# Kernel optimization log

Hardware: AMD Instinct MI355X
Metric: run time of the kernel (lower is better)

Reference implementation:

```python
import jax, jax.numpy as jnp
import numpy as np

IOU_THR = 0.5
NEG_POS = 3
CONF_W = 1.0
LOC_W = 1.0


def setup_inputs() -> dict:
    key = jax.random.key(0)
    ks = jax.random.split(key, 6)
    B, A, G = 16, 65536, 32
    ac = jax.random.uniform(ks[0], (B, A, 2))
    asz = jax.random.uniform(ks[1], (B, A, 2)) * 0.28 + 0.02
    anchors = jnp.concatenate([ac - asz / 2, ac + asz / 2], -1)
    gc = jax.random.uniform(ks[2], (B, G, 2))
    gsz = jax.random.uniform(ks[3], (B, G, 2)) * 0.28 + 0.02
    gt_boxes = jnp.concatenate([gc - gsz / 2, gc + gsz / 2], -1)
    bbox_pred = anchors + 0.05 * jax.random.normal(ks[4], (B, A, 4))
    # probabilities strictly inside (0,1) for BCE
    conf_pred = jax.random.uniform(ks[5], (B, A)) * 0.98 + 0.01
    return {"bbox_pred": bbox_pred, "conf_pred": conf_pred,
            "anchors": anchors, "gt_boxes": gt_boxes}


def _box_iou(a, g):
    # a: [A,4] xyxy, g: [G,4] xyxy -> [A,G]
    lt = jnp.maximum(a[:, None, :2], g[None, :, :2])
    rb = jnp.minimum(a[:, None, 2:], g[None, :, 2:])
    wh = jnp.clip(rb - lt, 0.0)
    inter = wh[..., 0] * wh[..., 1]
    area_a = (a[:, 2] - a[:, 0]) * (a[:, 3] - a[:, 1])
    area_g = (g[:, 2] - g[:, 0]) * (g[:, 3] - g[:, 1])
    return inter / (area_a[:, None] + area_g[None, :] - inter)


def _bce(p, t):
    return -(t * jnp.log(p) + (1.0 - t) * jnp.log1p(-p))


def _smooth_l1(x):
    ax = jnp.abs(x)
    return jnp.where(ax < 1.0, 0.5 * ax * ax, ax - 0.5)


def _per_image(bp, cp, an, gt):
    # bp: [A,4] pred boxes, cp: [A] conf, an: [A,4] anchors, gt: [G,4]
    A = cp.shape[0]
    ious = _box_iou(an, gt)                      # [A,G]
    best_gt_iou = ious.max(1)                    # [A]
    best_gt_idx = ious.argmax(1)                 # [A]
    best_anchor_idx = ious.argmax(0)             # [G] force-match each gt
    mask = (best_gt_iou > IOU_THR).at[best_anchor_idx].set(True)
    num_pos = mask.sum()

    # localization loss (center/size parameterization), summed over positives
    matched = gt[best_gt_idx]                    # [A,4]
    pc = (bp[:, :2] + bp[:, 2:]) / 2
    ps = bp[:, 2:] - bp[:, :2]
    gc = (matched[:, :2] + matched[:, 2:]) / 2
    gs = matched[:, 2:] - matched[:, :2]
    loc = _smooth_l1(jnp.concatenate([pc, ps], 1) - jnp.concatenate([gc, gs], 1)).sum(1)
    loc_loss = jnp.where(mask, loc, 0.0).sum()

    # confidence loss with hard negative mining
    t = mask.astype(cp.dtype)
    bce = _bce(cp, t)
    pos_loss = jnp.where(mask, bce, 0.0).sum()
    neg_bce = jnp.where(mask, 0.0, bce)
    num_neg = jnp.minimum(num_pos * NEG_POS, A - num_pos)
    sorted_neg = -jnp.sort(-neg_bce)             # descending
    neg_loss = jnp.where(jnp.arange(A) < num_neg, sorted_neg, 0.0).sum()
    conf_loss = pos_loss / jnp.maximum(num_pos, 1) + neg_loss / jnp.maximum(num_neg, 1)
    return loc_loss, conf_loss, num_pos


def reference(bbox_pred, conf_pred, anchors, gt_boxes):
    loc, conf, npos = jax.vmap(_per_image)(bbox_pred, conf_pred, anchors, gt_boxes)
    B = bbox_pred.shape[0]
    total_npos = jnp.maximum(npos.sum(), 1)
    total_loc = loc.sum() / total_npos * LOC_W
    total_conf = conf.sum() / B * CONF_W
    return total_loc + total_conf
```

## Files before the change

### kernel.cpp

```cpp
#include <hip/hip_runtime.h>

#define BB 16
#define AA 65536
#define GG 32
#define NB 8192
#define KOFF 59904u
#define AT 4
#define APB (256 * AT)
#define MBLK (AA / APB)
#define NSEG 16
#define SEGA (AA / NSEG)

__device__ unsigned char      g_mask[(size_t)BB * AA];
__device__ unsigned char      g_bidx[(size_t)BB * AA];
__device__ unsigned long long g_fpart[(size_t)BB * GG * MBLK];
__device__ unsigned int       g_hpart[(size_t)BB * NSEG * (NB/2)];
__device__ float g_spart[BB * NSEG * 2];
__device__ int   g_npart[BB * NSEG];
__device__ float g_loc[BB], g_pos[BB], g_neg[BB];
__device__ int   g_npos[BB], g_nneg[BB];
__device__ int   g_done;

__device__ __forceinline__ float midval(int bin) {
    return __uint_as_float((((unsigned int)bin + KOFF) << 14) | 8192u);
}

__global__ void __launch_bounds__(256, 4)
k_matchforce(const float4* __restrict__ anchors,
             const float4* __restrict__ gts) {
    __shared__ float4 sg[GG];
    __shared__ unsigned long long wkey[4][GG];
    const int b = blockIdx.y;
    const int t = threadIdx.x;
    const int wave = t >> 6, lane = t & 63;
    if (blockIdx.x == 0 && b == 0 && t == 0) g_done = 0;
    if (t < GG) sg[t] = gts[(size_t)b * GG + t];
    __syncthreads();

    const size_t abase = (size_t)b * AA + (size_t)blockIdx.x * APB;

    float ax0[AT], ay0[AT], ax1[AT], ay1[AT], aar[AT], best[AT];
    int bg[AT];
#pragma unroll
    for (int j = 0; j < AT; ++j) {
        const float4 av = anchors[abase + j * 256 + t];
        ax0[j] = av.x; ay0[j] = av.y; ax1[j] = av.z; ay1[j] = av.w;
        aar[j] = (av.z - av.x) * (av.w - av.y);
        best[j] = -1.0f; bg[j] = 0;
    }

#pragma unroll 2
    for (int g = 0; g < GG; ++g) {
        const float4 gb = sg[g];
        const float ga = (gb.z - gb.x) * (gb.w - gb.y);
        float fbest = -1.0f;
        int fo = t;
#pragma unroll
        for (int j = 0; j < AT; ++j) {
            const float lx = fmaxf(ax0[j], gb.x), ly = fmaxf(ay0[j], gb.y);
            const float rx = fminf(ax1[j], gb.z), ry = fminf(ay1[j], gb.w);
            const float w = fmaxf(rx - lx, 0.0f), h = fmaxf(ry - ly, 0.0f);
            const float inter = w * h;
            const float s = aar[j] + ga;
            const float r = inter * __builtin_amdgcn_rcpf(s);
            if (r > best[j]) { best[j] = r; bg[j] = g; }
            if (r > fbest)   { fbest = r; fo = j * 256 + t; }
        }
        unsigned long long key =
            ((unsigned long long)__float_as_uint(fbest) << 32) |
            (unsigned long long)(0xFFFFFFFFu - (unsigned int)fo);
#pragma unroll
        for (int off = 1; off < 64; off <<= 1) {
            const unsigned long long o = __shfl_xor(key, off, 64);
            if (o > key) key = o;
        }
        if (lane == 0) wkey[wave][g] = key;
    }

#pragma unroll
    for (int j = 0; j < AT; ++j) {
        g_mask[abase + j * 256 + t] = (best[j] > (1.0f / 3.0f)) ? 1 : 0;
        g_bidx[abase + j * 256 + t] = (unsigned char)bg[j];
    }
    __syncthreads();
    if (t < GG) {
        unsigned long long k = wkey[0][t];
#pragma unroll
        for (int w = 1; w < 4; ++w) {
            const unsigned long long k1 = wkey[w][t];
            if (k1 > k) k = k1;
        }
        const unsigned int off = 0xFFFFFFFFu - (unsigned int)(k & 0xFFFFFFFFull);
        const unsigned int ga = (unsigned int)(blockIdx.x * APB) + off;
        g_fpart[((size_t)b * GG + t) * MBLK + blockIdx.x] =
            (k & 0xFFFFFFFF00000000ull) |
            (unsigned long long)(0xFFFFFFFFu - ga);
    }
}

__global__ void k_stats(const float4* __restrict__ bbox,
                        const float* __restrict__ conf,
                        const float4* __restrict__ gts) {
    __shared__ float4 sg[GG];
    __shared__ unsigned int hp[NB / 2];
    __shared__ unsigned int bmap[SEGA / 32];
    __shared__ float rf[256], rf2[256];
    __shared__ unsigned int ru[256];
    const int b = blockIdx.y, seg = blockIdx.x, t = threadIdx.x;
    if (t < GG) sg[t] = gts[(size_t)b * GG + t];
    for (int j = t; j < NB / 2; j += 256) hp[j] = 0u;
    if (t < SEGA / 32) bmap[t] = 0u;
    __syncthreads();

    {
        const int gg = t >> 3, p = t & 7;
        const unsigned long long* fp =
            &g_fpart[((size_t)b * GG + gg) * MBLK + p * 8];
        unsigned long long k = 0;
#pragma unroll
        for (int m = 0; m < 8; ++m) { const unsigned long long v = fp[m]; if (v > k) k = v; }
#pragma unroll
        for (int off = 1; off < 8; off <<= 1) {
            const unsigned long long o = __shfl_xor(k, off, 64);
            if (o > k) k = o;
        }
        if (p == 0) {
            const unsigned int a = 0xFFFFFFFFu - (unsigned int)(k & 0xFFFFFFFFull);
            const int la = (int)a - seg * SEGA;
            if (la >= 0 && la < SEGA) atomicOr(&bmap[la >> 5], 1u << (la & 31));
        }
    }
    __syncthreads();

    const size_t base = (size_t)b * AA + (size_t)seg * SEGA;
    const float4* c4 = (const float4*)(conf + base);
    const uchar4* m4 = (const uchar4*)(g_mask + base);
    const uchar4* x4 = (const uchar4*)(g_bidx + base);
    const float4* bb4 = bbox + base;

    float pos = 0.0f, loc = 0.0f;
    int np = 0;
#pragma unroll
    for (int j = 0; j < SEGA / 1024; ++j) {
        const int idx = j * 256 + t;
        const float4 p4 = c4[idx];
        const uchar4 mm = m4[idx];
        const uchar4 xx = x4[idx];
        const unsigned int bw = (bmap[idx >> 3] >> ((idx & 7) * 4)) & 0xFu;
        const float pv[4] = {p4.x, p4.y, p4.z, p4.w};
        const unsigned char mv[4] = {mm.x, mm.y, mm.z, mm.w};
        const unsigned char xv[4] = {xx.x, xx.y, xx.z, xx.w};
#pragma unroll
        for (int c = 0; c < 4; ++c) {
            const float p = pv[c];
            if (mv[c] | ((bw >> c) & 1u)) {
                np += 1;
                pos += -logf(p);
                const float4 bv = bb4[4 * idx + c];
                const float4 gb = sg[xv[c]];
                const float d0 = (bv.x + bv.z) * 0.5f - (gb.x + gb.z) * 0.5f;
                const float d1 = (bv.y + bv.w) * 0.5f - (gb.y + gb.w) * 0.5f;
                const float d2 = (bv.z - bv.x) - (gb.z - gb.x);
                const float d3 = (bv.w - bv.y) - (gb.w - gb.y);
                float ds[4] = {d0, d1, d2, d3};
#pragma unroll
                for (int q = 0; q < 4; ++q) {
                    float ax = fabsf(ds[q]);
                    loc += (ax < 1.0f) ? 0.5f * ax * ax : ax - 0.5f;
                }
            } else {
                const float nb = -log1pf(-p);
                int key = (int)(__float_as_uint(nb) >> 14) - (int)KOFF;
                key = key < 0 ? 0 : (key > NB - 1 ? NB - 1 : key);
                atomicAdd(&hp[key >> 1], 1u << ((key & 1) << 4));
            }
        }
    }
    ru[t] = (unsigned int)np; rf[t] = pos; rf2[t] = loc;
    __syncthreads();
    for (int w = 128; w > 0; w >>= 1) {
        if (t < w) { ru[t] += ru[t + w]; rf[t] += rf[t + w]; rf2[t] += rf2[t + w]; }
        __syncthreads();
    }
    if (t == 0) {
        g_npart[b * NSEG + seg] = (int)ru[0];
        g_spart[(b * NSEG + seg) * 2 + 0] = rf[0];
        g_spart[(b * NSEG + seg) * 2 + 1] = rf2[0];
    }
    unsigned int* outp = g_hpart + ((size_t)b * NSEG + seg) * (NB / 2);
    for (int j = t; j < NB / 2; j += 256) outp[j] = hp[j];
}

__global__ void __launch_bounds__(1024) k_select(unsigned int* __restrict__ out) {
    __shared__ unsigned int hist[NB];
    __shared__ unsigned int ru[1024];
    __shared__ unsigned int s2[32];
    __shared__ float sh_pos, sh_loc;
    __shared__ int sh_np, sh_k, sh_bsel;
    __shared__ unsigned int sh_take;
    __shared__ float rf[1024];

    const int b = blockIdx.x, t = threadIdx.x;
    for (int w = t; w < NB / 2; w += 1024) {
        unsigned int lo = 0, hi = 0;
#pragma unroll
        for (int s = 0; s < NSEG; ++s) {
            const unsigned int v = g_hpart[((size_t)b * NSEG + s) * (NB / 2) + w];
            lo += v & 0xFFFFu; hi += v >> 16;
        }
        hist[2 * w] = lo; hist[2 * w + 1] = hi;
    }
    if (t == 0) {
        int np = 0; float pos = 0.0f, loc = 0.0f;
        for (int s = 0; s < NSEG; ++s) {
            np += g_npart[b * NSEG + s];
            pos += g_spart[(b * NSEG + s) * 2 + 0];
            loc += g_spart[(b * NSEG + s) * 2 + 1];
        }
        sh_np = np; sh_pos = pos; sh_loc = loc;
    }
    __syncthreads();
    const int np_tot = sh_np;

    unsigned int c = 0;
    const int hi = NB - 1 - t * 8;
#pragma unroll
    for (int j = 0; j < 8; ++j) c += hist[hi - j];
    ru[t] = c;
    __syncthreads();
    if (t < 32) {
        unsigned int x = 0;
#pragma unroll
        for (int j = 0; j < 32; ++j) x += ru[t * 32 + j];
        s2[t] = x;
    }
    __syncthreads();
    if (t == 0) {
        int k = 3 * np_tot;
        const int maxneg = AA - np_tot;
        if (k > maxneg) k = maxneg;
        sh_k = k;
        int bsel = NB;
        unsigned int take = 0;
        if (k > 0) {
            unsigned int cum = 0;
            int u = 0;
            while (u < 31 && cum + s2[u] < (unsigned int)k) { cum += s2[u]; ++u; }
            int cc = u * 32;
            while (cc < 1023 && cum + ru[cc] < (unsigned int)k) { cum += ru[cc]; ++cc; }
            const int h2 = NB - 1 - cc * 8;
            int j = 0;
            while (j < 7 && cum + hist[h2 - j] < (unsigned int)k) { cum += hist[h2 - j]; ++j; }
            bsel = h2 - j;
            take = (unsigned int)k - cum;
        }
        sh_bsel = bsel; sh_take = take;
    }
    __syncthreads();
    const int bsel = sh_bsel;
    float negp = 0.0f;
    for (int j = t; j < NB; j += 1024)
        if (j > bsel) { unsigned int cnt = hist[j]; if (cnt) negp += (float)cnt * midval(j); }
    rf[t] = negp;
    __syncthreads();
    for (int w = 512; w > 0; w >>= 1) {
        if (t < w) rf[t] += rf[t + w];
        __syncthreads();
    }
    if (t == 0) {
        float neg = 0.0f;
        if (sh_k > 0) neg = rf[0] + (float)sh_take * midval(bsel < NB ? bsel : 0);
        g_loc[b] = sh_loc; g_pos[b] = sh_pos; g_neg[b] = neg;
        g_npos[b] = np_tot; g_nneg[b] = sh_k;

        __threadfence();
        const int old = atomicAdd(&g_done, 1);
        if (old == BB - 1) {
            __threadfence();
            float loc = 0.0f, conf = 0.0f;
            int tot = 0;
            for (int bb = 0; bb < BB; ++bb) {
                const float lv = __hip_atomic_load(&g_loc[bb],  __ATOMIC_RELAXED, __HIP_MEMORY_SCOPE_AGENT);
                const float pv = __hip_atomic_load(&g_pos[bb],  __ATOMIC_RELAXED, __HIP_MEMORY_SCOPE_AGENT);
                const float nv = __hip_atomic_load(&g_neg[bb],  __ATOMIC_RELAXED, __HIP_MEMORY_SCOPE_AGENT);
                const int   np = __hip_atomic_load(&g_npos[bb], __ATOMIC_RELAXED, __HIP_MEMORY_SCOPE_AGENT);
                const int   nn = __hip_atomic_load(&g_nneg[bb], __ATOMIC_RELAXED, __HIP_MEMORY_SCOPE_AGENT);
                loc += lv;
                conf += pv / (float)(np > 1 ? np : 1) +
                        nv / (float)(nn > 1 ? nn : 1);
                tot += np;
            }
            const float total = loc / (float)(tot > 1 ? tot : 1) + conf / (float)BB;
            const unsigned int u = __float_as_uint(total);
            const unsigned int r = 0x7FFFu + ((u >> 16) & 1u);
            const unsigned int bf = (u + r) >> 16;
            out[0] = (bf << 16) | bf;
        }
    }
}

extern "C" void kernel_launch(void* const* d_in, const int* in_sizes, int n_in,
                              void* d_out, int out_size, void* d_ws, size_t ws_size,
                              hipStream_t stream) {
    const float4* bbox    = (const float4*)d_in[0];
    const float*  conf    = (const float*)d_in[1];
    const float4* anchors = (const float4*)d_in[2];
    const float4* gts     = (const float4*)d_in[3];

    k_matchforce<<<dim3(MBLK, BB), 256, 0, stream>>>(anchors, gts);
    k_stats<<<dim3(NSEG, BB), 256, 0, stream>>>(bbox, conf, gts);
    k_select<<<BB, 1024, 0, stream>>>((unsigned int*)d_out);
}
```

Measured before the change: 132.1 us.

## Accumulate histograms and force-match keys with global atomics, widen stats grid

Replaces the per-segment partial histograms and the per-block force-match key partials with per-image global buffers that are updated by atomicAdd and atomicMax. The buffers are zeroed by a memset issued before the kernels. k_stats now uses 64 segments, one element group per thread, instead of 16 segments with a loop, which gives more parallelism. k_select reads one finished histogram per image instead of reducing 16 partials. The aim is to remove the large partial-histogram writes and reads, at the cost of contended global atomics and an extra memset launch.

```diff
diff --git a/kernel.cpp b/kernel.cpp
--- a/kernel.cpp
+++ b/kernel.cpp
@@ -8,18 +8,27 @@
 #define AT 4
 #define APB (256 * AT)
 #define MBLK (AA / APB)
-#define NSEG 16
+#define NSEG 64
 #define SEGA (AA / NSEG)
 
-__device__ unsigned char      g_mask[(size_t)BB * AA];
-__device__ unsigned char      g_bidx[(size_t)BB * AA];
-__device__ unsigned long long g_fpart[(size_t)BB * GG * MBLK];
-__device__ unsigned int       g_hpart[(size_t)BB * NSEG * (NB/2)];
+__device__ unsigned char g_mask[(size_t)BB * AA];
+__device__ unsigned char g_bidx[(size_t)BB * AA];
 __device__ float g_spart[BB * NSEG * 2];
 __device__ int   g_npart[BB * NSEG];
 __device__ float g_loc[BB], g_pos[BB], g_neg[BB];
 __device__ int   g_npos[BB], g_nneg[BB];
-__device__ int   g_done;
+
+#define DYN_U32 (BB * NB + BB * GG * 2 + 2)
+__device__ unsigned int g_dyn[DYN_U32];
+__device__ __forceinline__ unsigned int* histp(int b) {
+    return g_dyn + (size_t)b * NB;
+}
+__device__ __forceinline__ unsigned long long* fkeyp() {
+    return (unsigned long long*)(g_dyn + BB * NB);
+}
+__device__ __forceinline__ int* donep() {
+    return (int*)(g_dyn + BB * NB + BB * GG * 2);
+}
 
 __device__ __forceinline__ float midval(int bin) {
     return __uint_as_float((((unsigned int)bin + KOFF) << 14) | 8192u);
@@ -33,7 +42,6 @@
     const int b = blockIdx.y;
     const int t = threadIdx.x;
     const int wave = t >> 6, lane = t & 63;
-    if (blockIdx.x == 0 && b == 0 && t == 0) g_done = 0;
     if (t < GG) sg[t] = gts[(size_t)b * GG + t];
     __syncthreads();
 
@@ -92,9 +100,9 @@
         }
         const unsigned int off = 0xFFFFFFFFu - (unsigned int)(k & 0xFFFFFFFFull);
         const unsigned int ga = (unsigned int)(blockIdx.x * APB) + off;
-        g_fpart[((size_t)b * GG + t) * MBLK + blockIdx.x] =
-            (k & 0xFFFFFFFF00000000ull) |
-            (unsigned long long)(0xFFFFFFFFu - ga);
+        atomicMax(&fkeyp()[b * GG + t],
+                  (k & 0xFFFFFFFF00000000ull) |
+                  (unsigned long long)(0xFFFFFFFFu - ga));
     }
 }
 
@@ -102,33 +110,18 @@
                         const float* __restrict__ conf,
                         const float4* __restrict__ gts) {
     __shared__ float4 sg[GG];
-    __shared__ unsigned int hp[NB / 2];
     __shared__ unsigned int bmap[SEGA / 32];
     __shared__ float rf[256], rf2[256];
     __shared__ unsigned int ru[256];
     const int b = blockIdx.y, seg = blockIdx.x, t = threadIdx.x;
     if (t < GG) sg[t] = gts[(size_t)b * GG + t];
-    for (int j = t; j < NB / 2; j += 256) hp[j] = 0u;
     if (t < SEGA / 32) bmap[t] = 0u;
     __syncthreads();
-
-    {
-        const int gg = t >> 3, p = t & 7;
-        const unsigned long long* fp =
-            &g_fpart[((size_t)b * GG + gg) * MBLK + p * 8];
-        unsigned long long k = 0;
-#pragma unroll
-        for (int m = 0; m < 8; ++m) { const unsigned long long v = fp[m]; if (v > k) k = v; }
-#pragma unroll
-        for (int off = 1; off < 8; off <<= 1) {
-            const unsigned long long o = __shfl_xor(k, off, 64);
-            if (o > k) k = o;
-        }
-        if (p == 0) {
-            const unsigned int a = 0xFFFFFFFFu - (unsigned int)(k & 0xFFFFFFFFull);
-            const int la = (int)a - seg * SEGA;
-            if (la >= 0 && la < SEGA) atomicOr(&bmap[la >> 5], 1u << (la & 31));
-        }
+    if (t < GG) {
+        const unsigned long long k = fkeyp()[b * GG + t];
+        const unsigned int a = 0xFFFFFFFFu - (unsigned int)(k & 0xFFFFFFFFull);
+        const int la = (int)a - seg * SEGA;
+        if (la >= 0 && la < SEGA) atomicOr(&bmap[la >> 5], 1u << (la & 31));
     }
     __syncthreads();
 
@@ -137,12 +130,12 @@
     const uchar4* m4 = (const uchar4*)(g_mask + base);
     const uchar4* x4 = (const uchar4*)(g_bidx + base);
     const float4* bb4 = bbox + base;
+    unsigned int* hb = histp(b);
 
     float pos = 0.0f, loc = 0.0f;
     int np = 0;
-#pragma unroll
-    for (int j = 0; j < SEGA / 1024; ++j) {
-        const int idx = j * 256 + t;
+    {
+        const int idx = t;
         const float4 p4 = c4[idx];
         const uchar4 mm = m4[idx];
         const uchar4 xx = x4[idx];
@@ -172,7 +165,7 @@
                 const float nb = -log1pf(-p);
                 int key = (int)(__float_as_uint(nb) >> 14) - (int)KOFF;
                 key = key < 0 ? 0 : (key > NB - 1 ? NB - 1 : key);
-                atomicAdd(&hp[key >> 1], 1u << ((key & 1) << 4));
+                atomicAdd(&hb[key], 1u);
             }
         }
     }
@@ -187,8 +180,6 @@
         g_spart[(b * NSEG + seg) * 2 + 0] = rf[0];
         g_spart[(b * NSEG + seg) * 2 + 1] = rf2[0];
     }
-    unsigned int* outp = g_hpart + ((size_t)b * NSEG + seg) * (NB / 2);
-    for (int j = t; j < NB / 2; j += 256) outp[j] = hp[j];
 }
 
 __global__ void __launch_bounds__(1024) k_select(unsigned int* __restrict__ out) {
@@ -201,23 +192,27 @@
     __shared__ float rf[1024];
 
     const int b = blockIdx.x, t = threadIdx.x;
-    for (int w = t; w < NB / 2; w += 1024) {
-        unsigned int lo = 0, hi = 0;
-#pragma unroll
-        for (int s = 0; s < NSEG; ++s) {
-            const unsigned int v = g_hpart[((size_t)b * NSEG + s) * (NB / 2) + w];
-            lo += v & 0xFFFFu; hi += v >> 16;
-        }
-        hist[2 * w] = lo; hist[2 * w + 1] = hi;
-    }
-    if (t == 0) {
-        int np = 0; float pos = 0.0f, loc = 0.0f;
-        for (int s = 0; s < NSEG; ++s) {
-            np += g_npart[b * NSEG + s];
-            pos += g_spart[(b * NSEG + s) * 2 + 0];
-            loc += g_spart[(b * NSEG + s) * 2 + 1];
-        }
-        sh_np = np; sh_pos = pos; sh_loc = loc;
+    {
+        const uint4* h4 = (const uint4*)histp(b);
+#pragma unroll
+        for (int w = 0; w < 2; ++w) {
+            const int i = w * 1024 + t;
+            const uint4 v = h4[i];
+            hist[4 * i + 0] = v.x; hist[4 * i + 1] = v.y;
+            hist[4 * i + 2] = v.z; hist[4 * i + 3] = v.w;
+        }
+    }
+    if (t < 64) {
+        int np = g_npart[b * NSEG + t];
+        float pos = g_spart[(b * NSEG + t) * 2 + 0];
+        float loc = g_spart[(b * NSEG + t) * 2 + 1];
+#pragma unroll
+        for (int off = 32; off > 0; off >>= 1) {
+            np  += __shfl_xor(np,  off, 64);
+            pos += __shfl_xor(pos, off, 64);
+            loc += __shfl_xor(loc, off, 64);
+        }
+        if (t == 0) { sh_np = np; sh_pos = pos; sh_loc = loc; }
     }
     __syncthreads();
     const int np_tot = sh_np;
@@ -274,7 +269,7 @@
         g_npos[b] = np_tot; g_nneg[b] = sh_k;
 
         __threadfence();
-        const int old = atomicAdd(&g_done, 1);
+        const int old = atomicAdd(donep(), 1);
         if (old == BB - 1) {
             __threadfence();
             float loc = 0.0f, conf = 0.0f;
@@ -307,6 +302,10 @@
     const float4* anchors = (const float4*)d_in[2];
     const float4* gts     = (const float4*)d_in[3];
 
+    static unsigned int* dynp = nullptr;
+    if (!dynp) hipGetSymbolAddress((void**)&dynp, HIP_SYMBOL(g_dyn));
+    hipMemsetAsync(dynp, 0, sizeof(unsigned int) * DYN_U32, stream);
+
     k_matchforce<<<dim3(MBLK, BB), 256, 0, stream>>>(anchors, gts);
     k_stats<<<dim3(NSEG, BB), 256, 0, stream>>>(bbox, conf, gts);
     k_select<<<BB, 1024, 0, stream>>>((unsigned int*)d_out);
```

New measurement: 231.0 us. 1.75x slower.
